# Kernel tuning notes

Hardware: AMD Instinct MI355X
Metric: run time of the kernel (lower is better)

The kernel has to match this reference:

```python
import jax, jax.numpy as jnp
import numpy as np
from jax import lax

N = 400000
INC = 128
MIDC = 64
OUTC = 128
KVOL = 27
EPS = 1e-5


def _bn(h, g, b, m, v):
    return (h - m) * (g * lax.rsqrt(v + EPS)) + b


def setup_inputs() -> dict:
    key = jax.random.key(0)
    ks = jax.random.split(key, 16)
    x = jax.random.normal(ks[0], (N, INC), jnp.float32)
    nb = jax.random.randint(ks[1], (KVOL, N), 0, N, jnp.int32)
    s1 = 1.0 / np.sqrt(INC)
    s2 = 1.0 / np.sqrt(MIDC * KVOL)
    s3 = 1.0 / np.sqrt(MIDC)
    w1 = jax.random.normal(ks[2], (INC, MIDC), jnp.float32) * s1
    w2 = jax.random.normal(ks[3], (KVOL, MIDC, MIDC), jnp.float32) * s2
    w3 = jax.random.normal(ks[4], (MIDC, OUTC), jnp.float32) * s3
    def bn_params(k, c):
        k1, k2, k3, k4 = jax.random.split(k, 4)
        return (jax.random.normal(k1, (c,), jnp.float32) * 0.1 + 1.0,
                jax.random.normal(k2, (c,), jnp.float32) * 0.1,
                jax.random.normal(k3, (c,), jnp.float32) * 0.1,
                jax.random.uniform(k4, (c,), jnp.float32) + 0.5)
    bn1_g, bn1_b, bn1_m, bn1_v = bn_params(ks[5], MIDC)
    bn2_g, bn2_b, bn2_m, bn2_v = bn_params(ks[6], MIDC)
    bn3_g, bn3_b, bn3_m, bn3_v = bn_params(ks[7], OUTC)
    return dict(x=x, nb=nb, w1=w1, w2=w2, w3=w3,
                bn1_g=bn1_g, bn1_b=bn1_b, bn1_m=bn1_m, bn1_v=bn1_v,
                bn2_g=bn2_g, bn2_b=bn2_b, bn2_m=bn2_m, bn2_v=bn2_v,
                bn3_g=bn3_g, bn3_b=bn3_b, bn3_m=bn3_m, bn3_v=bn3_v)


def reference(x, nb, w1, w2, w3,
              bn1_g, bn1_b, bn1_m, bn1_v,
              bn2_g, bn2_b, bn2_m, bn2_v,
              bn3_g, bn3_b, bn3_m, bn3_v):
    # 1x1 sparse conv == pointwise matmul
    h = jax.nn.relu(_bn(x @ w1, bn1_g, bn1_b, bn1_m, bn1_v))  # [N, midc]

    # ks=3 sparse conv: gather-matmul-accumulate over 27 kernel offsets
    def body(acc, kw):
        idx, wk = kw  # idx: [N] gather indices, wk: [midc, midc]
        return acc + h[idx] @ wk, None
    acc0 = jnp.zeros((N, MIDC), h.dtype)
    h2, _ = lax.scan(body, acc0, (nb, w2))
    h2 = jax.nn.relu(_bn(h2, bn2_g, bn2_b, bn2_m, bn2_v))

    # 1x1 conv + BN, then residual add (identity downsample: inc==outc, stride==1)
    h3 = _bn(h2 @ w3, bn3_g, bn3_b, bn3_m, bn3_v)  # [N, outc]
    return jax.nn.relu(h3 + x)
```

## Files before the change

kernel.cpp:

```cpp
#include <hip/hip_runtime.h>

#define N_PTS 400000
#define EPS 1e-5f

typedef __attribute__((ext_vector_type(8))) short short8;
typedef __attribute__((ext_vector_type(4))) float f32x4;

constexpr size_t H_OFF   = 0;
constexpr size_t W1T_OFF = 51200000;
constexpr size_t W2S_OFF = W1T_OFF + 16384;
constexpr size_t W3T_OFF = W2S_OFF + 221184;
constexpr size_t BNC_OFF = W3T_OFF + 16384;

__device__ __forceinline__ short f2bf(float f) {
  unsigned u = __builtin_bit_cast(unsigned, f);
  u += 0x7FFFu + ((u >> 16) & 1u);
  return (short)(u >> 16);
}

__global__ __launch_bounds__(256) void prep_kernel(
    const float* __restrict__ w1, const float* __restrict__ w2,
    const float* __restrict__ w3,
    const float* __restrict__ g1, const float* __restrict__ b1,
    const float* __restrict__ m1, const float* __restrict__ v1,
    const float* __restrict__ g2, const float* __restrict__ b2,
    const float* __restrict__ m2, const float* __restrict__ v2,
    const float* __restrict__ g3, const float* __restrict__ b3,
    const float* __restrict__ m3, const float* __restrict__ v3,
    short* __restrict__ w1t, short* __restrict__ w2s,
    short* __restrict__ w3t, float* __restrict__ bnc) {
  int tid = blockIdx.x * 256 + threadIdx.x;
  int gs = gridDim.x * 256;
  for (int i = tid; i < 128 * 64; i += gs) {
    int k = i >> 6, n = i & 63;
    w1t[n * 128 + k] = f2bf(w1[i]);
  }
  for (int i = tid; i < 27 * 64 * 64; i += gs) {
    int kk = i >> 12, r = i & 4095, k = r >> 6, n = r & 63;
    int byte = (n * 64 + k) * 2;
    byte ^= (n & 7) << 4;
    w2s[kk * 4096 + (byte >> 1)] = f2bf(w2[i]);
  }
  for (int i = tid; i < 64 * 128; i += gs) {
    int k = i >> 7, n = i & 127;
    w3t[n * 64 + k] = f2bf(w3[i]);
  }
  if (tid < 64) {
    float s = g1[tid] * rsqrtf(v1[tid] + EPS);
    bnc[tid] = s; bnc[64 + tid] = b1[tid] - m1[tid] * s;
  } else if (tid < 128) {
    int c = tid - 64;
    float s = g2[c] * rsqrtf(v2[c] + EPS);
    bnc[128 + c] = s; bnc[192 + c] = b2[c] - m2[c] * s;
  } else if (tid < 256) {
    int c = tid - 128;
    float s = g3[c] * rsqrtf(v3[c] + EPS);
    bnc[256 + c] = s; bnc[384 + c] = b3[c] - m3[c] * s;
  }
}

__global__ __launch_bounds__(256) void stage1_kernel(
    const float* __restrict__ x, const short* __restrict__ w1t,
    const float* __restrict__ bnc, short* __restrict__ h) {
  const int lane = threadIdx.x & 63;
  const int wid = threadIdx.x >> 6;
  const int lr = lane & 15, lk = lane >> 4;
  const long wbase = ((long)blockIdx.x * 4 + wid) * 64;
  if (wbase >= N_PTS) return;

  short8 bf[4][4];
#pragma unroll
  for (int nf = 0; nf < 4; ++nf)
#pragma unroll
    for (int ks = 0; ks < 4; ++ks)
      bf[nf][ks] = *(const short8*)(w1t + (nf * 16 + lr) * 128 + ks * 32 + lk * 8);

  float s[4], t[4];
#pragma unroll
  for (int nf = 0; nf < 4; ++nf) {
    int ch = nf * 16 + lr;
    s[nf] = bnc[ch]; t[nf] = bnc[64 + ch];
  }

#pragma unroll
  for (int mt = 0; mt < 4; ++mt) {
    f32x4 acc[4];
#pragma unroll
    for (int nf = 0; nf < 4; ++nf) acc[nf] = f32x4{0.f, 0.f, 0.f, 0.f};
    const float* xr = x + (wbase + mt * 16 + lr) * 128 + lk * 8;
#pragma unroll
    for (int ks = 0; ks < 4; ++ks) {
      f32x4 lo = *(const f32x4*)(xr + ks * 32);
      f32x4 hi = *(const f32x4*)(xr + ks * 32 + 4);
      short8 a;
#pragma unroll
      for (int j = 0; j < 4; ++j) { a[j] = f2bf(lo[j]); a[4 + j] = f2bf(hi[j]); }
#pragma unroll
      for (int nf = 0; nf < 4; ++nf)
        acc[nf] = __builtin_amdgcn_mfma_f32_16x16x32_bf16(a, bf[nf][ks], acc[nf], 0, 0, 0);
    }
    short* hr = h + (wbase + mt * 16) * 64;
#pragma unroll
    for (int nf = 0; nf < 4; ++nf) {
      int ch = nf * 16 + lr;
#pragma unroll
      for (int j = 0; j < 4; ++j) {
        int row = lk * 4 + j;
        float v = acc[nf][j] * s[nf] + t[nf];
        v = v > 0.f ? v : 0.f;
        hr[row * 64 + ch] = f2bf(v);
      }
    }
  }
}

__global__ __launch_bounds__(256, 4) void stage23_kernel(
    const short* __restrict__ h, const int* __restrict__ nb,
    const short* __restrict__ w2s, const short* __restrict__ w3t,
    const float* __restrict__ bnc, const float* __restrict__ x,
    float* __restrict__ out) {
  __shared__ __align__(16) short bbuf[2][4096];
  __shared__ __align__(16) short tile[4][16][72];
  const int tid = threadIdx.x;
  const int lane = tid & 63;
  const int wid = tid >> 6;
  const int lr = lane & 15, lk = lane >> 4;
  const long wbase = ((long)blockIdx.x * 4 + wid) * 32;

  int boff[4][2];
#pragma unroll
  for (int nf = 0; nf < 4; ++nf) {
    int row = nf * 16 + lr;
#pragma unroll
    for (int ks = 0; ks < 2; ++ks)
      boff[nf][ks] = ((row * 128 + ks * 64 + lk * 16) ^ ((row & 7) << 4)) >> 1;
  }

  f32x4 acc[2][4];
#pragma unroll
  for (int mt = 0; mt < 2; ++mt)
#pragma unroll
    for (int nf = 0; nf < 4; ++nf) acc[mt][nf] = f32x4{0.f, 0.f, 0.f, 0.f};

  int idxq[4][2];
#pragma unroll
  for (int kk = 0; kk < 3; ++kk)
#pragma unroll
    for (int mt = 0; mt < 2; ++mt)
      idxq[kk][mt] = nb[(long)kk * N_PTS + wbase + mt * 16 + lr];

  short8 acur[2][2], anext[2][2];
#pragma unroll
  for (int mt = 0; mt < 2; ++mt)
#pragma unroll
    for (int ks = 0; ks < 2; ++ks)
      acur[mt][ks] = *(const short8*)(h + (long)idxq[0][mt] * 64 + ks * 32 + lk * 8);

  {
    short8 b0a = *(const short8*)(w2s + tid * 16);
    short8 b0b = *(const short8*)(w2s + tid * 16 + 8);
    short8 b1a = *(const short8*)(w2s + 4096 + tid * 16);
    short8 b1b = *(const short8*)(w2s + 4096 + tid * 16 + 8);
    *(short8*)(&bbuf[0][tid * 16]) = b0a;
    *(short8*)(&bbuf[0][tid * 16 + 8]) = b0b;
    *(short8*)(&bbuf[1][tid * 16]) = b1a;
    *(short8*)(&bbuf[1][tid * 16 + 8]) = b1b;
  }
  asm volatile("s_waitcnt lgkmcnt(0)" ::: "memory");
  __builtin_amdgcn_s_barrier();

#pragma unroll
  for (int k = 0; k < 27; ++k) {
    const int kp = k & 1;
    short8 bsa, bsb;
    if (k + 2 < 27) {
      bsa = *(const short8*)(w2s + (k + 2) * 4096 + tid * 16);
      bsb = *(const short8*)(w2s + (k + 2) * 4096 + tid * 16 + 8);
    }
    if (k + 3 < 27) {
#pragma unroll
      for (int mt = 0; mt < 2; ++mt)
        idxq[(k + 3) & 3][mt] = nb[(long)(k + 3) * N_PTS + wbase + mt * 16 + lr];
    }
    if (k + 1 < 27) {
#pragma unroll
      for (int mt = 0; mt < 2; ++mt)
#pragma unroll
        for (int ks = 0; ks < 2; ++ks)
          anext[mt][ks] = *(const short8*)(h + (long)idxq[(k + 1) & 3][mt] * 64 + ks * 32 + lk * 8);
    }
#pragma unroll
    for (int nf = 0; nf < 4; ++nf) {
#pragma unroll
      for (int ks = 0; ks < 2; ++ks) {
        short8 bf = *(const short8*)(&bbuf[kp][boff[nf][ks]]);
#pragma unroll
        for (int mt = 0; mt < 2; ++mt)
          acc[mt][nf] = __builtin_amdgcn_mfma_f32_16x16x32_bf16(acur[mt][ks], bf, acc[mt][nf], 0, 0, 0);
      }
    }
    asm volatile("s_waitcnt lgkmcnt(0)" ::: "memory");
    __builtin_amdgcn_s_barrier();
    if (k + 2 < 27) {
      *(short8*)(&bbuf[kp][tid * 16]) = bsa;
      *(short8*)(&bbuf[kp][tid * 16 + 8]) = bsb;
    }
    if (k + 1 < 27) {
#pragma unroll
      for (int mt = 0; mt < 2; ++mt)
#pragma unroll
        for (int ks = 0; ks < 2; ++ks)
          acur[mt][ks] = anext[mt][ks];
    }
  }

  float s2[4], t2[4];
#pragma unroll
  for (int nf = 0; nf < 4; ++nf) {
    int ch = nf * 16 + lr;
    s2[nf] = bnc[128 + ch]; t2[nf] = bnc[192 + ch];
  }

#pragma unroll
  for (int mt = 0; mt < 2; ++mt) {
#pragma unroll
    for (int nf = 0; nf < 4; ++nf) {
      int ch = nf * 16 + lr;
#pragma unroll
      for (int j = 0; j < 4; ++j) {
        float v = acc[mt][nf][j] * s2[nf] + t2[nf];
        v = v > 0.f ? v : 0.f;
        tile[wid][lk * 4 + j][ch] = f2bf(v);
      }
    }
    asm volatile("s_waitcnt lgkmcnt(0)" ::: "memory");
    __builtin_amdgcn_sched_barrier(0);

    f32x4 acc3[8];
#pragma unroll
    for (int nf = 0; nf < 8; ++nf) acc3[nf] = f32x4{0.f, 0.f, 0.f, 0.f};
#pragma unroll
    for (int ks = 0; ks < 2; ++ks) {
      short8 a3 = *(const short8*)&tile[wid][lr][ks * 32 + lk * 8];
#pragma unroll
      for (int nf = 0; nf < 8; ++nf) {
        short8 b3 = *(const short8*)(w3t + (nf * 16 + lr) * 64 + ks * 32 + lk * 8);
        acc3[nf] = __builtin_amdgcn_mfma_f32_16x16x32_bf16(a3, b3, acc3[nf], 0, 0, 0);
      }
    }
    __builtin_amdgcn_sched_barrier(0);

    const float* xr = x + (wbase + mt * 16 + lk * 4) * 128;
    float* outr = out + (wbase + mt * 16 + lk * 4) * 128;
#pragma unroll
    for (int nf = 0; nf < 8; ++nf) {
      int ch = nf * 16 + lr;
      float s3 = bnc[256 + ch], t3 = bnc[384 + ch];
#pragma unroll
      for (int j = 0; j < 4; ++j) {
        float v = acc3[nf][j] * s3 + t3 + xr[j * 128 + ch];
        outr[j * 128 + ch] = v > 0.f ? v : 0.f;
      }
    }
    __builtin_amdgcn_sched_barrier(0);
  }
}

extern "C" void kernel_launch(void* const* d_in, const int* in_sizes, int n_in,
                              void* d_out, int out_size, void* d_ws, size_t ws_size,
                              hipStream_t stream) {
  const float* x  = (const float*)d_in[0];
  const int*   nb = (const int*)d_in[1];
  const float* w1 = (const float*)d_in[2];
  const float* w2 = (const float*)d_in[3];
  const float* w3 = (const float*)d_in[4];
  const float* g1 = (const float*)d_in[5];
  const float* b1 = (const float*)d_in[6];
  const float* m1 = (const float*)d_in[7];
  const float* v1 = (const float*)d_in[8];
  const float* g2 = (const float*)d_in[9];
  const float* b2 = (const float*)d_in[10];
  const float* m2 = (const float*)d_in[11];
  const float* v2 = (const float*)d_in[12];
  const float* g3 = (const float*)d_in[13];
  const float* b3 = (const float*)d_in[14];
  const float* m3 = (const float*)d_in[15];
  const float* v3 = (const float*)d_in[16];

  char* ws = (char*)d_ws;
  short* hbuf = (short*)(ws + H_OFF);
  short* w1t  = (short*)(ws + W1T_OFF);
  short* w2s  = (short*)(ws + W2S_OFF);
  short* w3t  = (short*)(ws + W3T_OFF);
  float* bnc  = (float*)(ws + BNC_OFF);
  float* outp = (float*)d_out;

  prep_kernel<<<128, 256, 0, stream>>>(w1, w2, w3,
                                       g1, b1, m1, v1,
                                       g2, b2, m2, v2,
                                       g3, b3, m3, v3,
                                       w1t, w2s, w3t, bnc);
  stage1_kernel<<<1563, 256, 0, stream>>>(x, w1t, bnc, hbuf);
  stage23_kernel<<<3125, 256, 0, stream>>>(hbuf, nb, w2s, w3t, bnc, x, outp);
}
```

Before: 375.5 us.

## Deepen gather pipeline and process two kernel offsets per barrier

The 27-offset sparse-conv loop now processes two offsets per iteration with a 4-deep ring of LDS weight buffers and a 4-deep register ring of gathered activations, prefetching two offsets ahead. This halves the number of block barriers and keeps more random gathers in flight to hide their latency. The stage-3 tile reuses the weight buffer LDS after a final barrier, so total LDS stays about the same while register pressure rises from the larger prefetch ring, which could reduce occupancy under the 4-block launch bound.

```diff
diff --git a/kernel.cpp b/kernel.cpp
--- a/kernel.cpp
+++ b/kernel.cpp
@@ -119,8 +119,7 @@
     const short* __restrict__ w2s, const short* __restrict__ w3t,
     const float* __restrict__ bnc, const float* __restrict__ x,
     float* __restrict__ out) {
-  __shared__ __align__(16) short bbuf[2][4096];
-  __shared__ __align__(16) short tile[4][16][72];
+  __shared__ __align__(16) short bbuf[4][4096];
   const int tid = threadIdx.x;
   const int lane = tid & 63;
   const int wid = tid >> 6;
@@ -142,78 +141,115 @@
 #pragma unroll
     for (int nf = 0; nf < 4; ++nf) acc[mt][nf] = f32x4{0.f, 0.f, 0.f, 0.f};
 
+  const int* nb0 = nb + wbase + lr;
+
   int idxq[4][2];
-#pragma unroll
-  for (int kk = 0; kk < 3; ++kk)
+  short8 ag[4][2][2];
+  short8 bs[2][2];
+
+#pragma unroll
+  for (int kk = 0; kk < 4; ++kk)
 #pragma unroll
     for (int mt = 0; mt < 2; ++mt)
-      idxq[kk][mt] = nb[(long)kk * N_PTS + wbase + mt * 16 + lr];
-
-  short8 acur[2][2], anext[2][2];
-#pragma unroll
-  for (int mt = 0; mt < 2; ++mt)
-#pragma unroll
-    for (int ks = 0; ks < 2; ++ks)
-      acur[mt][ks] = *(const short8*)(h + (long)idxq[0][mt] * 64 + ks * 32 + lk * 8);
+      idxq[kk][mt] = nb0[(long)kk * N_PTS + mt * 16];
 
   {
-    short8 b0a = *(const short8*)(w2s + tid * 16);
-    short8 b0b = *(const short8*)(w2s + tid * 16 + 8);
-    short8 b1a = *(const short8*)(w2s + 4096 + tid * 16);
-    short8 b1b = *(const short8*)(w2s + 4096 + tid * 16 + 8);
-    *(short8*)(&bbuf[0][tid * 16]) = b0a;
-    *(short8*)(&bbuf[0][tid * 16 + 8]) = b0b;
-    *(short8*)(&bbuf[1][tid * 16]) = b1a;
-    *(short8*)(&bbuf[1][tid * 16 + 8]) = b1b;
-  }
+    bs[0][0] = *(const short8*)(w2s + tid * 16);
+    bs[0][1] = *(const short8*)(w2s + tid * 16 + 8);
+    bs[1][0] = *(const short8*)(w2s + 4096 + tid * 16);
+    bs[1][1] = *(const short8*)(w2s + 4096 + tid * 16 + 8);
+  }
+#pragma unroll
+  for (int kk = 0; kk < 2; ++kk)
+#pragma unroll
+    for (int mt = 0; mt < 2; ++mt)
+#pragma unroll
+      for (int ks = 0; ks < 2; ++ks)
+        ag[kk][mt][ks] = *(const short8*)(h + (long)idxq[kk][mt] * 64 + ks * 32 + lk * 8);
+
+  *(short8*)(&bbuf[0][tid * 16]) = bs[0][0];
+  *(short8*)(&bbuf[0][tid * 16 + 8]) = bs[0][1];
+  *(short8*)(&bbuf[1][tid * 16]) = bs[1][0];
+  *(short8*)(&bbuf[1][tid * 16 + 8]) = bs[1][1];
   asm volatile("s_waitcnt lgkmcnt(0)" ::: "memory");
   __builtin_amdgcn_s_barrier();
 
 #pragma unroll
-  for (int k = 0; k < 27; ++k) {
-    const int kp = k & 1;
-    short8 bsa, bsb;
-    if (k + 2 < 27) {
-      bsa = *(const short8*)(w2s + (k + 2) * 4096 + tid * 16);
-      bsb = *(const short8*)(w2s + (k + 2) * 4096 + tid * 16 + 8);
-    }
-    if (k + 3 < 27) {
+  for (int p = 0; p < 13; ++p) {
+    const int k0 = 2 * p, k1 = 2 * p + 1;
+    if (k0 + 2 < 27) {
+      bs[0][0] = *(const short8*)(w2s + (k0 + 2) * 4096 + tid * 16);
+      bs[0][1] = *(const short8*)(w2s + (k0 + 2) * 4096 + tid * 16 + 8);
+    }
+    if (k1 + 2 < 27) {
+      bs[1][0] = *(const short8*)(w2s + (k1 + 2) * 4096 + tid * 16);
+      bs[1][1] = *(const short8*)(w2s + (k1 + 2) * 4096 + tid * 16 + 8);
+    }
+    if (k0 + 4 < 27)
 #pragma unroll
       for (int mt = 0; mt < 2; ++mt)
-        idxq[(k + 3) & 3][mt] = nb[(long)(k + 3) * N_PTS + wbase + mt * 16 + lr];
-    }
-    if (k + 1 < 27) {
+        idxq[(k0 + 4) & 3][mt] = nb0[(long)(k0 + 4) * N_PTS + mt * 16];
+    if (k1 + 4 < 27)
 #pragma unroll
       for (int mt = 0; mt < 2; ++mt)
+        idxq[(k1 + 4) & 3][mt] = nb0[(long)(k1 + 4) * N_PTS + mt * 16];
+    if (k0 + 2 < 27)
+#pragma unroll
+      for (int mt = 0; mt < 2; ++mt)
 #pragma unroll
         for (int ks = 0; ks < 2; ++ks)
-          anext[mt][ks] = *(const short8*)(h + (long)idxq[(k + 1) & 3][mt] * 64 + ks * 32 + lk * 8);
-    }
-#pragma unroll
-    for (int nf = 0; nf < 4; ++nf) {
-#pragma unroll
-      for (int ks = 0; ks < 2; ++ks) {
-        short8 bf = *(const short8*)(&bbuf[kp][boff[nf][ks]]);
-#pragma unroll
-        for (int mt = 0; mt < 2; ++mt)
-          acc[mt][nf] = __builtin_amdgcn_mfma_f32_16x16x32_bf16(acur[mt][ks], bf, acc[mt][nf], 0, 0, 0);
-      }
+          ag[(k0 + 2) & 3][mt][ks] =
+              *(const short8*)(h + (long)idxq[(k0 + 2) & 3][mt] * 64 + ks * 32 + lk * 8);
+    if (k1 + 2 < 27)
+#pragma unroll
+      for (int mt = 0; mt < 2; ++mt)
+#pragma unroll
+        for (int ks = 0; ks < 2; ++ks)
+          ag[(k1 + 2) & 3][mt][ks] =
+              *(const short8*)(h + (long)idxq[(k1 + 2) & 3][mt] * 64 + ks * 32 + lk * 8);
+    __builtin_amdgcn_sched_barrier(0);
+#pragma unroll
+    for (int kq = 0; kq < 2; ++kq) {
+      const int k = 2 * p + kq;
+#pragma unroll
+      for (int nf = 0; nf < 4; ++nf) {
+#pragma unroll
+        for (int ks = 0; ks < 2; ++ks) {
+          short8 bf = *(const short8*)(&bbuf[k & 3][boff[nf][ks]]);
+#pragma unroll
+          for (int mt = 0; mt < 2; ++mt)
+            acc[mt][nf] = __builtin_amdgcn_mfma_f32_16x16x32_bf16(ag[k & 3][mt][ks], bf, acc[mt][nf], 0, 0, 0);
+        }
+      }
+    }
+    if (k0 + 2 < 27) {
+      *(short8*)(&bbuf[(k0 + 2) & 3][tid * 16]) = bs[0][0];
+      *(short8*)(&bbuf[(k0 + 2) & 3][tid * 16 + 8]) = bs[0][1];
+    }
+    if (k1 + 2 < 27) {
+      *(short8*)(&bbuf[(k1 + 2) & 3][tid * 16]) = bs[1][0];
+      *(short8*)(&bbuf[(k1 + 2) & 3][tid * 16 + 8]) = bs[1][1];
     }
     asm volatile("s_waitcnt lgkmcnt(0)" ::: "memory");
     __builtin_amdgcn_s_barrier();
-    if (k + 2 < 27) {
-      *(short8*)(&bbuf[kp][tid * 16]) = bsa;
-      *(short8*)(&bbuf[kp][tid * 16 + 8]) = bsb;
-    }
-    if (k + 1 < 27) {
-#pragma unroll
-      for (int mt = 0; mt < 2; ++mt)
-#pragma unroll
-        for (int ks = 0; ks < 2; ++ks)
-          acur[mt][ks] = anext[mt][ks];
-    }
-  }
-
+  }
+  {
+    const int k = 26;
+#pragma unroll
+    for (int nf = 0; nf < 4; ++nf) {
+#pragma unroll
+      for (int ks = 0; ks < 2; ++ks) {
+        short8 bf = *(const short8*)(&bbuf[k & 3][boff[nf][ks]]);
+#pragma unroll
+        for (int mt = 0; mt < 2; ++mt)
+          acc[mt][nf] = __builtin_amdgcn_mfma_f32_16x16x32_bf16(ag[k & 3][mt][ks], bf, acc[mt][nf], 0, 0, 0);
+      }
+    }
+  }
+  asm volatile("s_waitcnt lgkmcnt(0)" ::: "memory");
+  __builtin_amdgcn_s_barrier();
+
+  short* tilew = ((short*)bbuf) + wid * (16 * 72);
   float s2[4], t2[4];
 #pragma unroll
   for (int nf = 0; nf < 4; ++nf) {
@@ -230,7 +266,7 @@
       for (int j = 0; j < 4; ++j) {
         float v = acc[mt][nf][j] * s2[nf] + t2[nf];
         v = v > 0.f ? v : 0.f;
-        tile[wid][lk * 4 + j][ch] = f2bf(v);
+        tilew[(lk * 4 + j) * 72 + ch] = f2bf(v);
       }
     }
     asm volatile("s_waitcnt lgkmcnt(0)" ::: "memory");
@@ -241,7 +277,7 @@
     for (int nf = 0; nf < 8; ++nf) acc3[nf] = f32x4{0.f, 0.f, 0.f, 0.f};
 #pragma unroll
     for (int ks = 0; ks < 2; ++ks) {
-      short8 a3 = *(const short8*)&tile[wid][lr][ks * 32 + lk * 8];
+      short8 a3 = *(const short8*)&tilew[lr * 72 + ks * 32 + lk * 8];
 #pragma unroll
       for (int nf = 0; nf < 8; ++nf) {
         short8 b3 = *(const short8*)(w3t + (nf * 16 + lr) * 64 + ks * 32 + lk * 8);
```

Result: slower. 655.3 us (+74.5%).

## Split fused stage2/3 kernel into separate gather-conv and pointwise-conv kernels

Applied to the files above, without the earlier changes.

Unfuses the sparse 3x3 gather-matmul from the final 1x1 conv, residual add and ReLU. The intermediate h2 is written to a new bf16 workspace buffer and a new stage3 kernel reads it back. The aim is to free the gather kernel's registers and LDS so more waves can hide gather latency, and to give stage3 a denser per-wave layout of 64 rows with w3 fragments kept in registers. The cost is an extra round trip of about 51 MB through global memory plus one more kernel launch.

```diff
diff --git a/kernel.cpp b/kernel.cpp
--- a/kernel.cpp
+++ b/kernel.cpp
@@ -7,7 +7,8 @@
 typedef __attribute__((ext_vector_type(4))) float f32x4;
 
 constexpr size_t H_OFF   = 0;
-constexpr size_t W1T_OFF = 51200000;
+constexpr size_t H2_OFF  = 51200000;
+constexpr size_t W1T_OFF = 102400000;
 constexpr size_t W2S_OFF = W1T_OFF + 16384;
 constexpr size_t W3T_OFF = W2S_OFF + 221184;
 constexpr size_t BNC_OFF = W3T_OFF + 16384;
@@ -114,13 +115,11 @@
   }
 }
 
-__global__ __launch_bounds__(256, 4) void stage23_kernel(
+__global__ __launch_bounds__(256, 4) void stage2_kernel(
     const short* __restrict__ h, const int* __restrict__ nb,
-    const short* __restrict__ w2s, const short* __restrict__ w3t,
-    const float* __restrict__ bnc, const float* __restrict__ x,
-    float* __restrict__ out) {
+    const short* __restrict__ w2s, const float* __restrict__ bnc,
+    short* __restrict__ h2) {
   __shared__ __align__(16) short bbuf[2][4096];
-  __shared__ __align__(16) short tile[4][16][72];
   const int tid = threadIdx.x;
   const int lane = tid & 63;
   const int wid = tid >> 6;
@@ -142,14 +141,17 @@
 #pragma unroll
     for (int nf = 0; nf < 4; ++nf) acc[mt][nf] = f32x4{0.f, 0.f, 0.f, 0.f};
 
+  const int* nb0 = nb + wbase + lr;
+
   int idxq[4][2];
+  short8 acur[2][2], anext[2][2];
+
 #pragma unroll
   for (int kk = 0; kk < 3; ++kk)
 #pragma unroll
     for (int mt = 0; mt < 2; ++mt)
-      idxq[kk][mt] = nb[(long)kk * N_PTS + wbase + mt * 16 + lr];
-
-  short8 acur[2][2], anext[2][2];
+      idxq[kk][mt] = nb0[(long)kk * N_PTS + mt * 16];
+
 #pragma unroll
   for (int mt = 0; mt < 2; ++mt)
 #pragma unroll
@@ -180,7 +182,7 @@
     if (k + 3 < 27) {
 #pragma unroll
       for (int mt = 0; mt < 2; ++mt)
-        idxq[(k + 3) & 3][mt] = nb[(long)(k + 3) * N_PTS + wbase + mt * 16 + lr];
+        idxq[(k + 3) & 3][mt] = nb0[(long)(k + 3) * N_PTS + mt * 16];
     }
     if (k + 1 < 27) {
 #pragma unroll
@@ -223,6 +225,7 @@
 
 #pragma unroll
   for (int mt = 0; mt < 2; ++mt) {
+    short* h2r = h2 + (wbase + mt * 16) * 64;
 #pragma unroll
     for (int nf = 0; nf < 4; ++nf) {
       int ch = nf * 16 + lr;
@@ -230,25 +233,44 @@
       for (int j = 0; j < 4; ++j) {
         float v = acc[mt][nf][j] * s2[nf] + t2[nf];
         v = v > 0.f ? v : 0.f;
-        tile[wid][lk * 4 + j][ch] = f2bf(v);
+        h2r[(lk * 4 + j) * 64 + ch] = f2bf(v);
       }
     }
-    asm volatile("s_waitcnt lgkmcnt(0)" ::: "memory");
-    __builtin_amdgcn_sched_barrier(0);
+  }
+}
+
+__global__ __launch_bounds__(256) void stage3_kernel(
+    const short* __restrict__ h2, const short* __restrict__ w3t,
+    const float* __restrict__ bnc, const float* __restrict__ x,
+    float* __restrict__ out) {
+  const int lane = threadIdx.x & 63;
+  const int wid = threadIdx.x >> 6;
+  const int lr = lane & 15, lk = lane >> 4;
+  const long wbase = ((long)blockIdx.x * 4 + wid) * 64;
+  if (wbase >= N_PTS) return;
+
+  short8 b3[8][2];
+#pragma unroll
+  for (int nf = 0; nf < 8; ++nf)
+#pragma unroll
+    for (int ks = 0; ks < 2; ++ks)
+      b3[nf][ks] = *(const short8*)(w3t + (nf * 16 + lr) * 64 + ks * 32 + lk * 8);
+
+#pragma unroll
+  for (int mt = 0; mt < 4; ++mt) {
+    short8 a3[2];
+#pragma unroll
+    for (int ks = 0; ks < 2; ++ks)
+      a3[ks] = *(const short8*)(h2 + (wbase + mt * 16 + lr) * 64 + ks * 32 + lk * 8);
 
     f32x4 acc3[8];
 #pragma unroll
     for (int nf = 0; nf < 8; ++nf) acc3[nf] = f32x4{0.f, 0.f, 0.f, 0.f};
 #pragma unroll
-    for (int ks = 0; ks < 2; ++ks) {
-      short8 a3 = *(const short8*)&tile[wid][lr][ks * 32 + lk * 8];
-#pragma unroll
-      for (int nf = 0; nf < 8; ++nf) {
-        short8 b3 = *(const short8*)(w3t + (nf * 16 + lr) * 64 + ks * 32 + lk * 8);
-        acc3[nf] = __builtin_amdgcn_mfma_f32_16x16x32_bf16(a3, b3, acc3[nf], 0, 0, 0);
-      }
-    }
-    __builtin_amdgcn_sched_barrier(0);
+    for (int ks = 0; ks < 2; ++ks)
+#pragma unroll
+      for (int nf = 0; nf < 8; ++nf)
+        acc3[nf] = __builtin_amdgcn_mfma_f32_16x16x32_bf16(a3[ks], b3[nf][ks], acc3[nf], 0, 0, 0);
 
     const float* xr = x + (wbase + mt * 16 + lk * 4) * 128;
     float* outr = out + (wbase + mt * 16 + lk * 4) * 128;
@@ -262,7 +284,6 @@
         outr[j * 128 + ch] = v > 0.f ? v : 0.f;
       }
     }
-    __builtin_amdgcn_sched_barrier(0);
   }
 }
 
@@ -288,12 +309,13 @@
   const float* v3 = (const float*)d_in[16];
 
   char* ws = (char*)d_ws;
-  short* hbuf = (short*)(ws + H_OFF);
-  short* w1t  = (short*)(ws + W1T_OFF);
-  short* w2s  = (short*)(ws + W2S_OFF);
-  short* w3t  = (short*)(ws + W3T_OFF);
-  float* bnc  = (float*)(ws + BNC_OFF);
-  float* outp = (float*)d_out;
+  short* hbuf  = (short*)(ws + H_OFF);
+  short* h2buf = (short*)(ws + H2_OFF);
+  short* w1t   = (short*)(ws + W1T_OFF);
+  short* w2s   = (short*)(ws + W2S_OFF);
+  short* w3t   = (short*)(ws + W3T_OFF);
+  float* bnc   = (float*)(ws + BNC_OFF);
+  float* outp  = (float*)d_out;
 
   prep_kernel<<<128, 256, 0, stream>>>(w1, w2, w3,
                                        g1, b1, m1, v1,
@@ -301,5 +323,6 @@
                                        g3, b3, m3, v3,
                                        w1t, w2s, w3t, bnc);
   stage1_kernel<<<1563, 256, 0, stream>>>(x, w1t, bnc, hbuf);
-  stage23_kernel<<<3125, 256, 0, stream>>>(hbuf, nb, w2s, w3t, bnc, x, outp);
-}
+  stage2_kernel<<<3125, 256, 0, stream>>>(hbuf, nb, w2s, bnc, h2buf);
+  stage3_kernel<<<1563, 256, 0, stream>>>(h2buf, w3t, bnc, x, outp);
+}
```

Measured after the change: 389.6 us. +3.7%, slower.
